# Kernel optimization log

Hardware: AMD Instinct MI355X
Metric: run time of the kernel (lower is better)

Reference implementation:

```python
import jax, jax.numpy as jnp
import numpy as np

EPS = 1e-6

def _rms_norm(x, w):
    # RMSNorm over last dim (head_dim)
    var = jnp.mean(jnp.square(x), axis=-1, keepdims=True)
    return x * jax.lax.rsqrt(var + EPS) * w

def _apply_rope(x, cos, sin):
    # x: [b, s, h, d]; cos/sin: [s, d]. Interleaved (real, imag) pairs as in
    # diffusers apply_rotary_emb (use_real_unbind_dim=-1) used by Flux.
    xr = x[..., 0::2]
    xi = x[..., 1::2]
    rotated = jnp.stack([-xi, xr], axis=-1).reshape(x.shape)
    cs = cos[None, :, None, :]
    sn = sin[None, :, None, :]
    return x * cs + rotated * sn

def setup_inputs() -> dict:
    key = jax.random.key(0)
    ks = jax.random.split(key, 10)
    b, s, dim, h, hd = 1, 2048, 3072, 24, 128
    inner = h * hd
    scale = 1.0 / np.sqrt(dim)
    x = jax.random.normal(ks[0], (b, s, dim), dtype=jnp.float32)
    # rope tables: proper cos/sin of log-spaced frequencies
    pos = jnp.arange(s, dtype=jnp.float32)[:, None]
    freqs = 1.0 / (10000.0 ** (jnp.arange(0, hd, 2, dtype=jnp.float32) / hd))
    angles = pos * freqs[None, :]                      # [s, hd/2]
    angles = jnp.repeat(angles, 2, axis=-1)            # [s, hd] interleaved pairs
    rope_cos = jnp.cos(angles)
    rope_sin = jnp.sin(angles)
    Wq = jax.random.normal(ks[1], (dim, inner), dtype=jnp.float32) * scale
    Wk = jax.random.normal(ks[2], (dim, inner), dtype=jnp.float32) * scale
    Wv = jax.random.normal(ks[3], (dim, inner), dtype=jnp.float32) * scale
    bq = jax.random.normal(ks[4], (inner,), dtype=jnp.float32) * 0.01
    bk = jax.random.normal(ks[5], (inner,), dtype=jnp.float32) * 0.01
    bv = jax.random.normal(ks[6], (inner,), dtype=jnp.float32) * 0.01
    gq = jnp.ones((hd,), dtype=jnp.float32)
    gk = jnp.ones((hd,), dtype=jnp.float32)
    return {"x": x, "rope_cos": rope_cos, "rope_sin": rope_sin,
            "Wq": Wq, "bq": bq, "Wk": Wk, "bk": bk, "Wv": Wv, "bv": bv,
            "gq": gq, "gk": gk}

def reference(x, rope_cos, rope_sin, Wq, bq, Wk, bk, Wv, bv, gq, gk):
    b, s, _ = x.shape
    h, hd = 24, 128
    q = (x @ Wq + bq).reshape(b, s, h, hd)
    k = (x @ Wk + bk).reshape(b, s, h, hd)
    v = (x @ Wv + bv).reshape(b, s, h, hd)
    q = _apply_rope(_rms_norm(q, gq), rope_cos, rope_sin)
    k = _apply_rope(_rms_norm(k, gk), rope_cos, rope_sin)
    scale = 1.0 / jnp.sqrt(jnp.asarray(hd, dtype=q.dtype))
    scores = jnp.einsum('bshd,bthd->bhst', q, k) * scale
    attn = jax.nn.softmax(scores, axis=-1)
    out = jnp.einsum('bhst,bthd->bshd', attn, v)
    return out.reshape(b, s, h * hd)
```

## Files before the change

kernel.cpp:

```cpp
#include <hip/hip_runtime.h>
#include <hip/hip_bf16.h>

typedef __attribute__((ext_vector_type(8))) short short8;
typedef __attribute__((ext_vector_type(4))) float f32x4;
typedef __attribute__((ext_vector_type(16))) float f32x16;

#define SEQ 2048
#define DIM 3072
#define NHEAD 24
#define HDIM 128

__device__ __forceinline__ unsigned short f2bf(float f) {
  unsigned int b = __float_as_uint(f);
  b += 0x7fffu + ((b >> 16) & 1u);
  return (unsigned short)(b >> 16);
}
__device__ __forceinline__ float bf2f(unsigned short u) {
  return __uint_as_float(((unsigned int)u) << 16);
}
__device__ __forceinline__ unsigned int pkbf(float a, float b) {
  __hip_bfloat162 h = __float22bfloat162_rn(make_float2(a, b));
  return *(unsigned int*)&h;
}

__device__ __forceinline__ void async16(const void* g, void* l) {
  __builtin_amdgcn_global_load_lds(
      (const __attribute__((address_space(1))) unsigned int*)g,
      (__attribute__((address_space(3))) unsigned int*)l, 16, 0, 0);
}

__global__ void k_cvt_x(const float* __restrict__ x, unsigned short* __restrict__ xb) {
  int idx = (blockIdx.x * 256 + threadIdx.x) * 8;
  float4 a = *(const float4*)(x + idx);
  float4 b = *(const float4*)(x + idx + 4);
  short8 o;
  o[0] = (short)f2bf(a.x); o[1] = (short)f2bf(a.y);
  o[2] = (short)f2bf(a.z); o[3] = (short)f2bf(a.w);
  o[4] = (short)f2bf(b.x); o[5] = (short)f2bf(b.y);
  o[6] = (short)f2bf(b.z); o[7] = (short)f2bf(b.w);
  *(short8*)(xb + idx) = o;
}

__device__ __forceinline__ void transpose_tile(const float* __restrict__ w,
                                               unsigned short* __restrict__ wt,
                                               int n0, int k0, int outRowBase, int t) {
  __shared__ unsigned short tile[64][68];
  int c4 = (t & 15) * 4;
  int r0 = t >> 4;
#pragma unroll
  for (int j = 0; j < 4; ++j) {
    int r = r0 + 16 * j;
    float4 v = *(const float4*)(w + (size_t)(k0 + r) * DIM + n0 + c4);
    ushort4 u;
    u.x = f2bf(v.x); u.y = f2bf(v.y); u.z = f2bf(v.z); u.w = f2bf(v.w);
    *(ushort4*)&tile[r][c4] = u;
  }
  __syncthreads();
#pragma unroll
  for (int j = 0; j < 4; ++j) {
    int nn = r0 + 16 * j;
    ushort4 u;
    u.x = tile[c4 + 0][nn]; u.y = tile[c4 + 1][nn];
    u.z = tile[c4 + 2][nn]; u.w = tile[c4 + 3][nn];
    *(ushort4*)(wt + (size_t)(outRowBase + n0 + nn) * DIM + k0 + c4) = u;
  }
}

__global__ __launch_bounds__(256) void k_transpose(const float* __restrict__ w,
                                                   unsigned short* __restrict__ wt) {
  transpose_tile(w, wt, blockIdx.x * 64, blockIdx.y * 64, 0, threadIdx.x);
}

__global__ __launch_bounds__(256) void k_transpose3(const float* __restrict__ w0,
                                                    const float* __restrict__ w1,
                                                    const float* __restrict__ w2,
                                                    unsigned short* __restrict__ wt) {
  const float* w = blockIdx.z == 0 ? w0 : (blockIdx.z == 1 ? w1 : w2);
  transpose_tile(w, wt, blockIdx.x * 64, blockIdx.y * 64, blockIdx.z * DIM, threadIdx.x);
}

__device__ __forceinline__ void gemm_tile(const unsigned short* __restrict__ xb,
                                          const unsigned short* __restrict__ wt,
                                          int bm, int bn, int t, f32x4 (&acc)[4][4],
                                          unsigned short* As, unsigned short* Bs) {
  int l = t & 63, w = t >> 6;
  int wr = w >> 1, wc = w & 1;
  int lr = l & 15, kc = l >> 4;
  const char* aB = (const char*)xb;
  const char* bB = (const char*)wt;
  char* asmB = (char*)As;
  char* bsmB = (char*)Bs;
  int sw = (lr & 7) << 4;

  for (int k0 = 0; k0 < DIM; k0 += 64) {
#pragma unroll
    for (int i = 0; i < 4; ++i) {
      int off = (t + 256 * i) * 16;
      int row = off >> 7;
      int cb = off & 127;
      int scb = cb ^ ((row & 7) << 4);
      async16(aB + ((size_t)(bm * 128 + row) * DIM + k0) * 2 + scb, asmB + off);
      async16(bB + ((size_t)(bn * 128 + row) * DIM + k0) * 2 + scb, bsmB + off);
    }
    __syncthreads();
#pragma unroll
    for (int kk = 0; kk < 2; ++kk) {
      short8 af[4], bf[4];
#pragma unroll
      for (int m = 0; m < 4; ++m)
        af[m] = *(const short8*)(asmB + (wr * 64 + m * 16 + lr) * 128 +
                                 ((kk * 64 + kc * 16) ^ sw));
#pragma unroll
      for (int n = 0; n < 4; ++n)
        bf[n] = *(const short8*)(bsmB + (wc * 64 + n * 16 + lr) * 128 +
                                 ((kk * 64 + kc * 16) ^ sw));
#pragma unroll
      for (int m = 0; m < 4; ++m)
#pragma unroll
        for (int n = 0; n < 4; ++n)
          acc[m][n] = __builtin_amdgcn_mfma_f32_16x16x32_bf16(af[m], bf[n], acc[m][n], 0, 0, 0);
    }
    __syncthreads();
  }
}

__global__ __launch_bounds__(256) void k_gemm(const unsigned short* __restrict__ xb,
                                              const unsigned short* __restrict__ wt,
                                              const float* __restrict__ bias,
                                              unsigned short* __restrict__ out,
                                              int vmode) {
  __shared__ unsigned short As[128 * 64];
  __shared__ unsigned short Bs[128 * 64];
  int t = threadIdx.x;
  int fid = blockIdx.x;
  int logical = (fid & 7) * 48 + (fid >> 3);
  int bm = logical & 15, bn = logical >> 4;

  f32x4 acc[4][4];
#pragma unroll
  for (int m = 0; m < 4; ++m)
#pragma unroll
    for (int n = 0; n < 4; ++n) acc[m][n] = (f32x4){0.f, 0.f, 0.f, 0.f};

  gemm_tile(xb, wt, bm, bn, t, acc, As, Bs);

  int l = t & 63, w = t >> 6;
  int wr = w >> 1, wc = w & 1;
  int lr = l & 15, lq = l >> 4;
  if (vmode) {
#pragma unroll
    for (int m = 0; m < 4; ++m)
#pragma unroll
      for (int n = 0; n < 4; ++n) {
        int gcol = bn * 128 + wc * 64 + n * 16 + lr;
        float bv = bias[gcol];
        int grow = bm * 128 + wr * 64 + m * 16 + lq * 4;
        ushort4 u;
        u.x = f2bf(acc[m][n][0] + bv);
        u.y = f2bf(acc[m][n][1] + bv);
        u.z = f2bf(acc[m][n][2] + bv);
        u.w = f2bf(acc[m][n][3] + bv);
        *(ushort4*)(out + (size_t)gcol * SEQ + grow) = u;
      }
  } else {
#pragma unroll
    for (int m = 0; m < 4; ++m)
#pragma unroll
      for (int n = 0; n < 4; ++n) {
        int gcol = bn * 128 + wc * 64 + n * 16 + lr;
        float bv = bias[gcol];
#pragma unroll
        for (int i = 0; i < 4; ++i) {
          int grow = bm * 128 + wr * 64 + m * 16 + lq * 4 + i;
          out[(size_t)grow * DIM + gcol] = f2bf(acc[m][n][i] + bv);
        }
      }
  }
}

__global__ __launch_bounds__(256) void k_gemm3(const unsigned short* __restrict__ xb,
                                               const unsigned short* __restrict__ wt,
                                               const float* __restrict__ bq,
                                               const float* __restrict__ bk,
                                               const float* __restrict__ bv,
                                               unsigned short* __restrict__ qb,
                                               unsigned short* __restrict__ kb,
                                               unsigned short* __restrict__ vtb) {
  __shared__ unsigned short As[128 * 64];
  __shared__ unsigned short Bs[128 * 64];
  int t = threadIdx.x;
  int fid = blockIdx.x;
  int logical = (fid & 7) * 144 + (fid >> 3);
  int bm = logical & 15, bn = logical >> 4;

  f32x4 acc[4][4];
#pragma unroll
  for (int m = 0; m < 4; ++m)
#pragma unroll
    for (int n = 0; n < 4; ++n) acc[m][n] = (f32x4){0.f, 0.f, 0.f, 0.f};

  gemm_tile(xb, wt, bm, bn, t, acc, As, Bs);

  int l = t & 63, w = t >> 6;
  int wr = w >> 1, wc = w & 1;
  int lr = l & 15, lq = l >> 4;

  int region = bn >= 48 ? 2 : (bn >= 24 ? 1 : 0);
  int bnl = bn - region * 24;
  const float* bias = region == 0 ? bq : (region == 1 ? bk : bv);

  if (region == 2) {
#pragma unroll
    for (int m = 0; m < 4; ++m)
#pragma unroll
      for (int n = 0; n < 4; ++n) {
        int gcol = bnl * 128 + wc * 64 + n * 16 + lr;
        float bv_ = bias[gcol];
        int grow = bm * 128 + wr * 64 + m * 16 + lq * 4;
        ushort4 u;
        u.x = f2bf(acc[m][n][0] + bv_);
        u.y = f2bf(acc[m][n][1] + bv_);
        u.z = f2bf(acc[m][n][2] + bv_);
        u.w = f2bf(acc[m][n][3] + bv_);
        *(ushort4*)(vtb + (size_t)gcol * SEQ + grow) = u;
      }
  } else {
    unsigned short* outp = region == 0 ? qb : kb;
#pragma unroll
    for (int m = 0; m < 4; ++m)
#pragma unroll
      for (int n = 0; n < 4; ++n) {
        int gcol = bnl * 128 + wc * 64 + n * 16 + lr;
        float bv_ = bias[gcol];
#pragma unroll
        for (int i = 0; i < 4; ++i) {
          int grow = bm * 128 + wr * 64 + m * 16 + lq * 4 + i;
          outp[(size_t)grow * DIM + gcol] = f2bf(acc[m][n][i] + bv_);
        }
      }
  }
}

__device__ __forceinline__ void normrope_row(unsigned short* __restrict__ buf, int row,
                                             const float* __restrict__ cosb,
                                             const float* __restrict__ sinb,
                                             const float* __restrict__ g, float scale, int l) {
  int s_idx = row / NHEAD, head = row % NHEAD;
  size_t base = (size_t)s_idx * DIM + head * HDIM;
  unsigned int pair = *(const unsigned int*)(buf + base + 2 * l);
  float x0 = bf2f((unsigned short)(pair & 0xffffu));
  float x1 = bf2f((unsigned short)(pair >> 16));
  float ss = x0 * x0 + x1 * x1;
#pragma unroll
  for (int off = 1; off < 64; off <<= 1) ss += __shfl_xor(ss, off);
  float r = rsqrtf(ss * (1.0f / 128.0f) + 1e-6f);
  float g0 = g[2 * l], g1 = g[2 * l + 1];
  float c0 = cosb[s_idx * HDIM + 2 * l], c1 = cosb[s_idx * HDIM + 2 * l + 1];
  float s0 = sinb[s_idx * HDIM + 2 * l], s1 = sinb[s_idx * HDIM + 2 * l + 1];
  float xn0 = x0 * r * g0, xn1 = x1 * r * g1;
  float o0 = (xn0 * c0 - xn1 * s0) * scale;
  float o1 = (xn1 * c1 + xn0 * s1) * scale;
  unsigned int po = (unsigned int)f2bf(o0) | ((unsigned int)f2bf(o1) << 16);
  *(unsigned int*)(buf + base + 2 * l) = po;
}

__global__ void k_normrope(unsigned short* __restrict__ qk, const float* __restrict__ cosb,
                           const float* __restrict__ sinb, const float* __restrict__ g,
                           float scale) {
  int t = threadIdx.x;
  normrope_row(qk, blockIdx.x * 4 + (t >> 6), cosb, sinb, g, scale, t & 63);
}

__global__ void k_normrope2(unsigned short* __restrict__ qb, unsigned short* __restrict__ kb,
                            const float* __restrict__ cosb, const float* __restrict__ sinb,
                            const float* __restrict__ gq, const float* __restrict__ gk) {
  int t = threadIdx.x;
  int row = blockIdx.x * 4 + (t >> 6);
  if (row < SEQ * NHEAD)
    normrope_row(qb, row, cosb, sinb, gq, 0.12751744f, t & 63);
  else
    normrope_row(kb, row - SEQ * NHEAD, cosb, sinb, gk, 1.0f, t & 63);
}

__global__ __launch_bounds__(128, 2) void k_attn(const unsigned short* __restrict__ q,
                                                 const unsigned short* __restrict__ k,
                                                 const unsigned short* __restrict__ vt,
                                                 float* __restrict__ out) {
  __shared__ unsigned short Ksm[64 * 128];
  __shared__ unsigned short Vtsm[128 * 64];
  int t = threadIdx.x;
  int w = t >> 6, l = t & 63;
  int q32 = l & 31, hi = l >> 5;
  int hi4 = hi * 4;
  int fid = blockIdx.x;
  int logical = (fid & 7) * 96 + (fid >> 3);
  int qt = logical & 31, h = logical >> 5;
  int q0w = qt * 64 + w * 32;

  const char* kbase = (const char*)k + (size_t)h * HDIM * 2;
  const char* vbase = (const char*)vt + (size_t)h * HDIM * SEQ * 2;

  int koff[8], voff[8];
#pragma unroll
  for (int i = 0; i < 8; ++i) {
    int off = (t + 128 * i) * 16;
    int krow = off >> 8, kcb = off & 255;
    koff[i] = krow * (DIM * 2) + (kcb ^ ((krow & 15) << 4));
    int vrow = off >> 7, vcb = off & 127;
    voff[i] = vrow * (SEQ * 2) + (vcb ^ ((vrow & 7) << 4));
  }

  short8 qf[8];
  {
    const unsigned short* qrow = q + (size_t)(q0w + q32) * DIM + h * HDIM;
#pragma unroll
    for (int ks = 0; ks < 8; ++ks) qf[ks] = *(const short8*)(qrow + ks * 16 + hi * 8);
  }

  f32x16 o0 = {0.f,0.f,0.f,0.f,0.f,0.f,0.f,0.f,0.f,0.f,0.f,0.f,0.f,0.f,0.f,0.f};
  f32x16 o1 = o0, o2 = o0, o3 = o0;
  float m_ = -1e30f, lsum = 0.f;
  int ksw = (q32 & 15) << 4;
  int vsw = (q32 & 7) << 4;

  union U8 { short8 s8; unsigned int u[4]; };

  for (int kt = 0; kt < 32; ++kt) {
    const char* kt_k = kbase + (size_t)kt * (64 * DIM * 2);
    const char* kt_v = vbase + kt * 128;
#pragma unroll
    for (int i = 0; i < 8; ++i) {
      int dst = (t + 128 * i) * 16;
      async16(kt_k + koff[i], (char*)Ksm + dst);
      async16(kt_v + voff[i], (char*)Vtsm + dst);
    }
    __syncthreads();

    f32x16 st0 = {0.f,0.f,0.f,0.f,0.f,0.f,0.f,0.f,0.f,0.f,0.f,0.f,0.f,0.f,0.f,0.f};
    f32x16 st1 = st0;
    {
      const char* kr0 = (const char*)Ksm + q32 * 256;
      const char* kr1 = (const char*)Ksm + (32 + q32) * 256;
      __builtin_amdgcn_s_setprio(1);
#pragma unroll
      for (int ks = 0; ks < 8; ++ks) {
        int cb = (ks * 32 + hi * 16) ^ ksw;
        short8 kf0 = *(const short8*)(kr0 + cb);
        short8 kf1 = *(const short8*)(kr1 + cb);
        st0 = __builtin_amdgcn_mfma_f32_32x32x16_bf16(kf0, qf[ks], st0, 0, 0, 0);
        st1 = __builtin_amdgcn_mfma_f32_32x32x16_bf16(kf1, qf[ks], st1, 0, 0, 0);
      }
      __builtin_amdgcn_s_setprio(0);
    }

    float mx = fmaxf(st0[0], st1[0]);
#pragma unroll
    for (int r = 1; r < 16; ++r) mx = fmaxf(mx, fmaxf(st0[r], st1[r]));
    mx = fmaxf(mx, __shfl_xor(mx, 32));

    if (__any(mx > m_ + 10.0f)) {
      float mn = fmaxf(m_, mx);
      float corr = exp2f(m_ - mn);
      m_ = mn;
      lsum *= corr;
#pragma unroll
      for (int r = 0; r < 16; ++r) {
        float cr = __shfl(corr, (r & 3) + 8 * (r >> 2) + hi4);
        o0[r] *= cr; o1[r] *= cr; o2[r] *= cr; o3[r] *= cr;
      }
    }

#pragma unroll
    for (int r = 0; r < 16; ++r) {
      st0[r] = exp2f(st0[r] - m_);
      st1[r] = exp2f(st1[r] - m_);
    }
    {
      float sm = st0[0] + st1[0];
#pragma unroll
      for (int r = 1; r < 16; ++r) sm += st0[r] + st1[r];
      sm += __shfl_xor(sm, 32);
      lsum += sm;
    }

    U8 pa[4];
#pragma unroll
    for (int b = 0; b < 4; ++b) {
      unsigned int a0, a1, a2, a3;
      if (b < 2) {
        int r0 = (b & 1) * 8;
        a0 = pkbf(st0[r0 + 0], st0[r0 + 1]);
        a1 = pkbf(st0[r0 + 2], st0[r0 + 3]);
        a2 = pkbf(st0[r0 + 4], st0[r0 + 5]);
        a3 = pkbf(st0[r0 + 6], st0[r0 + 7]);
      } else {
        int r0 = (b & 1) * 8;
        a0 = pkbf(st1[r0 + 0], st1[r0 + 1]);
        a1 = pkbf(st1[r0 + 2], st1[r0 + 3]);
        a2 = pkbf(st1[r0 + 4], st1[r0 + 5]);
        a3 = pkbf(st1[r0 + 6], st1[r0 + 7]);
      }
      asm volatile("v_permlane32_swap_b32 %0, %1" : "+v"(a0), "+v"(a2));
      asm volatile("v_permlane32_swap_b32 %0, %1" : "+v"(a1), "+v"(a3));
      pa[b].u[0] = a0; pa[b].u[1] = a1; pa[b].u[2] = a2; pa[b].u[3] = a3;
    }

    __builtin_amdgcn_s_setprio(1);
#pragma unroll
    for (int ks = 0; ks < 4; ++ks) {
      int cb = (ks * 32 + hi * 16) ^ vsw;
      short8 vf0 = *(const short8*)((const char*)Vtsm + (0 * 32 + q32) * 128 + cb);
      short8 vf1 = *(const short8*)((const char*)Vtsm + (1 * 32 + q32) * 128 + cb);
      short8 vf2 = *(const short8*)((const char*)Vtsm + (2 * 32 + q32) * 128 + cb);
      short8 vf3 = *(const short8*)((const char*)Vtsm + (3 * 32 + q32) * 128 + cb);
      o0 = __builtin_amdgcn_mfma_f32_32x32x16_bf16(pa[ks].s8, vf0, o0, 0, 0, 0);
      o1 = __builtin_amdgcn_mfma_f32_32x32x16_bf16(pa[ks].s8, vf1, o1, 0, 0, 0);
      o2 = __builtin_amdgcn_mfma_f32_32x32x16_bf16(pa[ks].s8, vf2, o2, 0, 0, 0);
      o3 = __builtin_amdgcn_mfma_f32_32x32x16_bf16(pa[ks].s8, vf3, o3, 0, 0, 0);
    }
    __builtin_amdgcn_s_setprio(0);

    __syncthreads();
  }

  float inv = 1.0f / lsum;
#pragma unroll
  for (int r = 0; r < 16; ++r) {
    float fr = __shfl(inv, (r & 3) + 8 * (r >> 2) + hi4);
    int grow = q0w + (r & 3) + 8 * (r >> 2) + hi4;
    float* orow = out + (size_t)grow * DIM + h * HDIM + q32;
    orow[0]  = o0[r] * fr;
    orow[32] = o1[r] * fr;
    orow[64] = o2[r] * fr;
    orow[96] = o3[r] * fr;
  }
}

extern "C" void kernel_launch(void* const* d_in, const int* in_sizes, int n_in,
                              void* d_out, int out_size, void* d_ws, size_t ws_size,
                              hipStream_t stream) {
  const float* x = (const float*)d_in[0];
  const float* rope_cos = (const float*)d_in[1];
  const float* rope_sin = (const float*)d_in[2];
  const float* Wq = (const float*)d_in[3];
  const float* bq = (const float*)d_in[4];
  const float* Wk = (const float*)d_in[5];
  const float* bk = (const float*)d_in[6];
  const float* Wv = (const float*)d_in[7];
  const float* bv = (const float*)d_in[8];
  const float* gq = (const float*)d_in[9];
  const float* gk = (const float*)d_in[10];
  float* out = (float*)d_out;

  const size_t slab = (size_t)SEQ * DIM;
  const size_t wt9elems = (size_t)3 * DIM * DIM;
  const size_t need = (4 * slab + wt9elems) * 2;

  if (ws_size >= need) {
    unsigned short* xb = (unsigned short*)d_ws;
    unsigned short* wt9 = xb + slab;
    unsigned short* qb = wt9 + wt9elems;
    unsigned short* kb = qb + slab;
    unsigned short* vtb = kb + slab;

    k_cvt_x<<<3072, 256, 0, stream>>>(x, xb);
    k_transpose3<<<dim3(DIM / 64, DIM / 64, 3), 256, 0, stream>>>(Wq, Wk, Wv, wt9);
    k_gemm3<<<1152, 256, 0, stream>>>(xb, wt9, bq, bk, bv, qb, kb, vtb);
    k_normrope2<<<2 * SEQ * NHEAD / 4, 256, 0, stream>>>(qb, kb, rope_cos, rope_sin, gq, gk);
    k_attn<<<768, 128, 0, stream>>>(qb, kb, vtb, out);
  } else {
    unsigned short* xb = (unsigned short*)d_ws;
    unsigned short* wt = xb + slab;
    unsigned short* qb = wt + (size_t)DIM * DIM;
    unsigned short* kb = qb + slab;
    unsigned short* vtb = kb + slab;

    k_cvt_x<<<3072, 256, 0, stream>>>(x, xb);
    dim3 tg(DIM / 64, DIM / 64);
    k_transpose<<<tg, 256, 0, stream>>>(Wq, wt);
    k_gemm<<<384, 256, 0, stream>>>(xb, wt, bq, qb, 0);
    k_transpose<<<tg, 256, 0, stream>>>(Wk, wt);
    k_gemm<<<384, 256, 0, stream>>>(xb, wt, bk, kb, 0);
    k_transpose<<<tg, 256, 0, stream>>>(Wv, wt);
    k_gemm<<<384, 256, 0, stream>>>(xb, wt, bv, vtb, 1);
    k_normrope<<<SEQ * NHEAD / 4, 256, 0, stream>>>(qb, rope_cos, rope_sin, gq, 0.12751744f);
    k_normrope<<<SEQ * NHEAD / 4, 256, 0, stream>>>(kb, rope_cos, rope_sin, gk, 1.0f);
    k_attn<<<768, 128, 0, stream>>>(qb, kb, vtb, out);
  }
}
```

Baseline: 317.9 us.

## Fuse RMSNorm and RoPE into the QKV GEMM epilogue

```diff
diff --git a/kernel.cpp b/kernel.cpp
--- a/kernel.cpp
+++ b/kernel.cpp
@@ -9,6 +9,7 @@
 #define DIM 3072
 #define NHEAD 24
 #define HDIM 128
+#define SCALE_Q 0.12751744f
 
 __device__ __forceinline__ unsigned short f2bf(float f) {
   unsigned int b = __float_as_uint(f);
@@ -178,20 +179,23 @@
   }
 }
 
-__global__ __launch_bounds__(256) void k_gemm3(const unsigned short* __restrict__ xb,
-                                               const unsigned short* __restrict__ wt,
-                                               const float* __restrict__ bq,
-                                               const float* __restrict__ bk,
-                                               const float* __restrict__ bv,
-                                               unsigned short* __restrict__ qb,
-                                               unsigned short* __restrict__ kb,
-                                               unsigned short* __restrict__ vtb) {
+__global__ __launch_bounds__(256, 4) void k_gemm3(
+    const unsigned short* __restrict__ xb, const unsigned short* __restrict__ wt,
+    const float* __restrict__ bq, const float* __restrict__ bk,
+    const float* __restrict__ bv, const float* __restrict__ rope_cos,
+    const float* __restrict__ rope_sin, const float* __restrict__ gq,
+    const float* __restrict__ gk, unsigned short* __restrict__ qb,
+    unsigned short* __restrict__ kb, unsigned short* __restrict__ vtb) {
   __shared__ unsigned short As[128 * 64];
   __shared__ unsigned short Bs[128 * 64];
+  __shared__ float ssum[2][128];
   int t = threadIdx.x;
   int fid = blockIdx.x;
-  int logical = (fid & 7) * 144 + (fid >> 3);
-  int bm = logical & 15, bn = logical >> 4;
+  int xcd = fid & 7, li = fid >> 3;
+  int c = li / 36, r = li % 36;
+  int bnl9 = r >> 2, bmi = r & 3;
+  int bm = c * 4 + bmi;
+  int bn = xcd * 9 + bnl9;
 
   f32x4 acc[4][4];
 #pragma unroll
@@ -226,28 +230,69 @@
       }
   } else {
     unsigned short* outp = region == 0 ? qb : kb;
+    const float* g = region == 0 ? gq : gk;
+    float scale = region == 0 ? SCALE_Q : 1.0f;
+
+    float gv[4], bvv[4];
+#pragma unroll
+    for (int n = 0; n < 4; ++n) {
+      int cl = wc * 64 + n * 16 + lr;
+      gv[n] = g[cl];
+      bvv[n] = bias[bnl * 128 + cl];
+    }
 #pragma unroll
     for (int m = 0; m < 4; ++m)
 #pragma unroll
-      for (int n = 0; n < 4; ++n) {
-        int gcol = bnl * 128 + wc * 64 + n * 16 + lr;
-        float bv_ = bias[gcol];
-#pragma unroll
-        for (int i = 0; i < 4; ++i) {
-          int grow = bm * 128 + wr * 64 + m * 16 + lq * 4 + i;
-          outp[(size_t)grow * DIM + gcol] = f2bf(acc[m][n][i] + bv_);
+      for (int n = 0; n < 4; ++n)
+#pragma unroll
+        for (int i = 0; i < 4; ++i) acc[m][n][i] += bvv[n];
+
+#pragma unroll
+    for (int m = 0; m < 4; ++m)
+#pragma unroll
+      for (int i = 0; i < 4; ++i) {
+        float ss = acc[m][0][i] * acc[m][0][i] + acc[m][1][i] * acc[m][1][i] +
+                   acc[m][2][i] * acc[m][2][i] + acc[m][3][i] * acc[m][3][i];
+        ss += __shfl_xor(ss, 1);
+        ss += __shfl_xor(ss, 2);
+        ss += __shfl_xor(ss, 4);
+        ss += __shfl_xor(ss, 8);
+        if (lr == m * 4 + i) ssum[wc][wr * 64 + m * 16 + lq * 4 + i] = ss;
+      }
+    __syncthreads();
+
+#pragma unroll
+    for (int m = 0; m < 4; ++m)
+#pragma unroll
+      for (int i = 0; i < 4; ++i) {
+        int rl = wr * 64 + m * 16 + lq * 4 + i;
+        float rn = rsqrtf((ssum[0][rl] + ssum[1][rl]) * (1.0f / 128.0f) + 1e-6f);
+        int s_idx = bm * 128 + rl;
+        const float* cr = rope_cos + (size_t)s_idx * HDIM;
+        const float* sr = rope_sin + (size_t)s_idx * HDIM;
+        unsigned short* orow = outp + (size_t)s_idx * DIM + bnl * 128;
+#pragma unroll
+        for (int n = 0; n < 4; ++n) {
+          int cl = wc * 64 + n * 16 + lr;
+          float xn = acc[m][n][i] * rn * gv[n];
+          float pr = __shfl_xor(xn, 1);
+          float cv = cr[cl], sv = sr[cl];
+          float o = (lr & 1) ? fmaf(xn, cv, pr * sv) : fmaf(xn, cv, -pr * sv);
+          orow[cl] = f2bf(o * scale);
         }
       }
   }
 }
 
-__device__ __forceinline__ void normrope_row(unsigned short* __restrict__ buf, int row,
-                                             const float* __restrict__ cosb,
-                                             const float* __restrict__ sinb,
-                                             const float* __restrict__ g, float scale, int l) {
+__global__ void k_normrope(unsigned short* __restrict__ qk, const float* __restrict__ cosb,
+                           const float* __restrict__ sinb, const float* __restrict__ g,
+                           float scale) {
+  int t = threadIdx.x;
+  int w = t >> 6, l = t & 63;
+  int row = blockIdx.x * 4 + w;
   int s_idx = row / NHEAD, head = row % NHEAD;
   size_t base = (size_t)s_idx * DIM + head * HDIM;
-  unsigned int pair = *(const unsigned int*)(buf + base + 2 * l);
+  unsigned int pair = *(const unsigned int*)(qk + base + 2 * l);
   float x0 = bf2f((unsigned short)(pair & 0xffffu));
   float x1 = bf2f((unsigned short)(pair >> 16));
   float ss = x0 * x0 + x1 * x1;
@@ -261,25 +306,7 @@
   float o0 = (xn0 * c0 - xn1 * s0) * scale;
   float o1 = (xn1 * c1 + xn0 * s1) * scale;
   unsigned int po = (unsigned int)f2bf(o0) | ((unsigned int)f2bf(o1) << 16);
-  *(unsigned int*)(buf + base + 2 * l) = po;
-}
-
-__global__ void k_normrope(unsigned short* __restrict__ qk, const float* __restrict__ cosb,
-                           const float* __restrict__ sinb, const float* __restrict__ g,
-                           float scale) {
-  int t = threadIdx.x;
-  normrope_row(qk, blockIdx.x * 4 + (t >> 6), cosb, sinb, g, scale, t & 63);
-}
-
-__global__ void k_normrope2(unsigned short* __restrict__ qb, unsigned short* __restrict__ kb,
-                            const float* __restrict__ cosb, const float* __restrict__ sinb,
-                            const float* __restrict__ gq, const float* __restrict__ gk) {
-  int t = threadIdx.x;
-  int row = blockIdx.x * 4 + (t >> 6);
-  if (row < SEQ * NHEAD)
-    normrope_row(qb, row, cosb, sinb, gq, 0.12751744f, t & 63);
-  else
-    normrope_row(kb, row - SEQ * NHEAD, cosb, sinb, gk, 1.0f, t & 63);
+  *(unsigned int*)(qk + base + 2 * l) = po;
 }
 
 __global__ __launch_bounds__(128, 2) void k_attn(const unsigned short* __restrict__ q,
@@ -465,8 +492,8 @@
 
     k_cvt_x<<<3072, 256, 0, stream>>>(x, xb);
     k_transpose3<<<dim3(DIM / 64, DIM / 64, 3), 256, 0, stream>>>(Wq, Wk, Wv, wt9);
-    k_gemm3<<<1152, 256, 0, stream>>>(xb, wt9, bq, bk, bv, qb, kb, vtb);
-    k_normrope2<<<2 * SEQ * NHEAD / 4, 256, 0, stream>>>(qb, kb, rope_cos, rope_sin, gq, gk);
+    k_gemm3<<<1152, 256, 0, stream>>>(xb, wt9, bq, bk, bv, rope_cos, rope_sin, gq, gk,
+                                      qb, kb, vtb);
     k_attn<<<768, 128, 0, stream>>>(qb, kb, vtb, out);
   } else {
     unsigned short* xb = (unsigned short*)d_ws;
@@ -483,7 +510,7 @@
     k_gemm<<<384, 256, 0, stream>>>(xb, wt, bk, kb, 0);
     k_transpose<<<tg, 256, 0, stream>>>(Wv, wt);
     k_gemm<<<384, 256, 0, stream>>>(xb, wt, bv, vtb, 1);
-    k_normrope<<<SEQ * NHEAD / 4, 256, 0, stream>>>(qb, rope_cos, rope_sin, gq, 0.12751744f);
+    k_normrope<<<SEQ * NHEAD / 4, 256, 0, stream>>>(qb, rope_cos, rope_sin, gq, SCALE_Q);
     k_normrope<<<SEQ * NHEAD / 4, 256, 0, stream>>>(kb, rope_cos, rope_sin, gk, 1.0f);
     k_attn<<<768, 128, 0, stream>>>(qb, kb, vtb, out);
   }
```

Result: faster. 286.8 us (-9.8%).
